# Kernel optimization log

Hardware: AMD Instinct MI355X
Metric: run time of the kernel (lower is better)

Reference implementation:

```python
import jax, jax.numpy as jnp
import numpy as np

BN_EPS = 1e-5


def _bn(x, g, b, m, v):
    # inference-mode BatchNorm2d over channel axis 1 of [B,C,F,T]
    scale = (g * jax.lax.rsqrt(v + BN_EPS))[None, :, None, None]
    shift = (b - g * m * jax.lax.rsqrt(v + BN_EPS))[None, :, None, None]
    return x * scale + shift


def _prelu(x, a):
    return jnp.where(x > 0, x, a[None, :, None, None] * x)


def _conv1x1(x, w):
    # w: [out, in]; x: [B,C,F,T]
    return jnp.einsum('oc,bcft->boft', w, x)


def setup_inputs() -> dict:
    key = jax.random.key(0)
    ks = jax.random.split(key, 8)
    B, C, F, T = 4, 64, 256, 400
    d_c = C // 4  # 16
    inp = jax.random.normal(ks[0], (B, C, F, T), dtype=jnp.float32)
    # causal time mask: True = masked (future frames)
    mask = jnp.triu(jnp.ones((T, T), dtype=bool), k=1)[None, None]  # [1,1,T,T]
    w_fqkv = jax.random.normal(ks[1], (3 * d_c, C), dtype=jnp.float32) / np.sqrt(C)
    w_tqk = jax.random.normal(ks[2], (2 * d_c, C), dtype=jnp.float32) / np.sqrt(C)
    w_proj = jax.random.normal(ks[3], (C, d_c), dtype=jnp.float32) / np.sqrt(d_c)
    def bn_params(k, n):
        k1, k2 = jax.random.split(k)
        return (1.0 + 0.1 * jax.random.normal(k1, (n,), dtype=jnp.float32),
                0.1 * jax.random.normal(k2, (n,), dtype=jnp.float32),
                0.1 * jax.random.normal(jax.random.fold_in(k, 7), (n,), dtype=jnp.float32),
                jnp.abs(1.0 + 0.1 * jax.random.normal(jax.random.fold_in(k, 9), (n,), dtype=jnp.float32)))
    g1, b1, m1, v1 = bn_params(ks[4], 3 * d_c)
    g2, b2, m2, v2 = bn_params(ks[5], 2 * d_c)
    g3, b3, m3, v3 = bn_params(ks[6], C)
    a1 = 0.25 * jnp.ones((3 * d_c,), dtype=jnp.float32)
    a2 = 0.25 * jnp.ones((2 * d_c,), dtype=jnp.float32)
    a3 = 0.25 * jnp.ones((C,), dtype=jnp.float32)
    return dict(inp=inp, mask=mask, w_fqkv=w_fqkv, g1=g1, b1=b1, m1=m1, v1=v1, a1=a1,
                w_tqk=w_tqk, g2=g2, b2=b2, m2=m2, v2=v2, a2=a2,
                w_proj=w_proj, g3=g3, b3=b3, m3=m3, v3=v3, a3=a3)


def reference(inp, mask, w_fqkv, g1, b1, m1, v1, a1,
              w_tqk, g2, b2, m2, v2, a2,
              w_proj, g3, b3, m3, v3, a3):
    d_c = w_proj.shape[1]
    scale = 1.0 / np.sqrt(d_c).astype(np.float32)
    # frequency attention
    f_qkv = _prelu(_bn(_conv1x1(inp, w_fqkv), g1, b1, m1, v1), a1)  # [B,3d,F,T]
    qf, kf, v = f_qkv[:, :d_c], f_qkv[:, d_c:2 * d_c], f_qkv[:, 2 * d_c:]
    f_score = jnp.einsum('bcft,bcyt->btfy', qf, kf) * scale
    f_score = jax.nn.softmax(f_score, axis=-1)
    f_out = jnp.einsum('btfy,bcyt->bcft', f_score, v)
    # time attention
    t_qk = _prelu(_bn(_conv1x1(inp, w_tqk), g2, b2, m2, v2), a2)  # [B,2d,F,T]
    qt, kt = t_qk[:, :d_c], t_qk[:, d_c:]
    t_score = jnp.einsum('bcft,bcfy->bfty', qt, kt) * scale
    neg = -jnp.finfo(t_score.dtype).max
    t_score = jnp.where(mask, neg, t_score)
    t_score = jax.nn.softmax(t_score, axis=-1)
    t_out = jnp.einsum('bfty,bcfy->bcft', t_score, f_out)
    out = _prelu(_bn(_conv1x1(t_out, w_proj), g3, b3, m3, v3), a3)
    return out + inp
```

## Files before the change

kernel.cpp:

```cpp
#include <hip/hip_runtime.h>
#include <hip/hip_bf16.h>

#define B_ 4
#define C_ 64
#define F_ 256
#define T_ 400
#define DC 16
#define NB 102400

typedef __hip_bfloat16 bf16;
typedef __attribute__((ext_vector_type(8))) short bf16x8s;
typedef __attribute__((ext_vector_type(4))) short short4v;
typedef __attribute__((ext_vector_type(4))) float f32x4;
typedef __attribute__((ext_vector_type(2))) short short2v;
typedef __attribute__((ext_vector_type(2))) unsigned int uint2v;
typedef __attribute__((ext_vector_type(4))) unsigned int uint4v;

__device__ __forceinline__ float b2f(bf16 x){ return __bfloat162float(x); }
__device__ __forceinline__ bf16  f2b(float x){ return __float2bfloat16(x); }
__device__ __forceinline__ short f2bs(float x){ bf16 h = __float2bfloat16(x); short s; __builtin_memcpy(&s,&h,2); return s; }

#define MFMA16(a,b,c) __builtin_amdgcn_mfma_f32_16x16x32_bf16((a),(b),(c),0,0,0)

__device__ __forceinline__ unsigned cvt_pk_bf16(float a, float b){
    unsigned r;
    asm("v_cvt_pk_bf16_f32 %0, %1, %2" : "=v"(r) : "v"(a), "v"(b));
    return r;
}
__device__ __forceinline__ void permlane32_swap(unsigned &a, unsigned &b){
    asm("v_permlane32_swap_b32 %0, %1" : "+v"(a), "+v"(b));
}
__device__ __forceinline__ void permlane16_swap(unsigned &a, unsigned &b){
    asm("v_permlane16_swap_b32 %0, %1" : "+v"(a), "+v"(b));
}

__global__ __launch_bounds__(256) void k_proj(
    const float* __restrict__ inp,
    const float* __restrict__ w_fqkv,
    const float* __restrict__ g1, const float* __restrict__ b1,
    const float* __restrict__ m1, const float* __restrict__ v1,
    const float* __restrict__ a1,
    const float* __restrict__ w_tqk,
    const float* __restrict__ g2, const float* __restrict__ b2,
    const float* __restrict__ m2, const float* __restrict__ v2,
    const float* __restrict__ a2,
    bf16* __restrict__ qf, bf16* __restrict__ kf, bf16* __restrict__ vv,
    bf16* __restrict__ qt, bf16* __restrict__ kt)
{
    __shared__ short Xs[256*64];
    __shared__ short Ws[80*72];
    __shared__ float sc[80], sh[80], al[80];

    const int tid = threadIdx.x;
    const int blk = blockIdx.x;
    const int b   = blk / 400;
    const int rem = blk - b*400;
    const int f0  = (rem & 15) * 16;
    const int t0  = (rem >> 4) * 16;

    for (int i = tid; i < 80*32; i += 256) {
        int o = i >> 5, cp = (i & 31) * 2;
        const float* src = (o < 48) ? &w_fqkv[o*64 + cp] : &w_tqk[(o-48)*64 + cp];
        short2v wv; wv.x = f2bs(src[0]); wv.y = f2bs(src[1]);
        *(short2v*)&Ws[o*72 + cp] = wv;
    }
    if (tid < 48) {
        float rs = rsqrtf(v1[tid] + 1e-5f);
        float g  = g1[tid];
        sc[tid] = g * rs;
        sh[tid] = b1[tid] - g * m1[tid] * rs;
        al[tid] = a1[tid];
    }
    if (tid >= 128 && tid < 160) {
        int o = tid - 128;
        float rs = rsqrtf(v2[o] + 1e-5f);
        float g  = g2[o];
        sc[48+o] = g * rs;
        sh[48+o] = b2[o] - g * m2[o] * rs;
        al[48+o] = a2[o];
    }
    {
        const int wv = tid >> 6, lnn = tid & 63;
        const int fi = lnn >> 2, tc = lnn & 3;
        const float* xb = inp + (size_t)b*64*NB + (size_t)(f0+fi)*T_ + t0 + tc*4;
        #pragma unroll
        for (int p = 0; p < 16; p++) {
            const int c = p*4 + wv;
            f32x4 x = *(const f32x4*)&xb[(size_t)c*NB];
            const int chi = c >> 3, clo = c & 7;
            #pragma unroll
            for (int j = 0; j < 4; j++) {
                int r = (tc*4 + j)*16 + fi;
                int slot = chi ^ (r & 7) ^ ((r >> 4) & 7);
                Xs[r*64 + slot*8 + clo] = f2bs(x[j]);
            }
        }
    }
    __syncthreads();

    const int wave = tid >> 6;
    const int lane = tid & 63;
    const int ln   = lane & 15;
    const int quad = lane >> 4;
    const f32x4 zero = {0.f,0.f,0.f,0.f};

    bf16x8s B1[4][2];
    bf16x8s B2[4][2];
    #pragma unroll
    for (int nt = 0; nt < 4; nt++) {
        const int tile = wave*4 + nt;
        {
            const int r  = tile*16 + ln;
            const int sw = (ln & 7) ^ (tile & 7);
            B1[nt][0] = *(const bf16x8s*)&Xs[r*64 + ((quad     ^ sw) * 8)];
            B1[nt][1] = *(const bf16x8s*)&Xs[r*64 + (((4+quad) ^ sw) * 8)];
        }
        {
            const int r  = ln*16 + tile;
            const int sw = (tile & 7) ^ (ln & 7);
            B2[nt][0] = *(const bf16x8s*)&Xs[r*64 + ((quad     ^ sw) * 8)];
            B2[nt][1] = *(const bf16x8s*)&Xs[r*64 + (((4+quad) ^ sw) * 8)];
        }
    }

    #pragma unroll
    for (int mt = 0; mt < 5; mt++) {
        bf16x8s A0 = *(const bf16x8s*)&Ws[(mt*16+ln)*72 + quad*8];
        bf16x8s A1 = *(const bf16x8s*)&Ws[(mt*16+ln)*72 + 32 + quad*8];
        float scv[4], shv[4], alv[4];
        #pragma unroll
        for (int r = 0; r < 4; r++) {
            int o = mt*16 + quad*4 + r;
            scv[r] = sc[o]; shv[r] = sh[o]; alv[r] = al[o];
        }
        #pragma unroll
        for (int nt = 0; nt < 4; nt++) {
            bf16x8s Bb0 = (mt < 3) ? B1[nt][0] : B2[nt][0];
            bf16x8s Bb1 = (mt < 3) ? B1[nt][1] : B2[nt][1];
            f32x4 acc = MFMA16(A0, Bb0, zero);
            acc = MFMA16(A1, Bb1, acc);
            short4v hs;
            #pragma unroll
            for (int r = 0; r < 4; r++) {
                float y = acc[r]*scv[r] + shv[r];
                y = y > 0.f ? y : alv[r]*y;
                if (mt == 0 || mt == 3) y *= 0.25f;
                hs[r] = f2bs(y);
            }
            const int tile = wave*4 + nt;
            if (mt < 3) {
                size_t idx = (((size_t)b*T_ + (t0+tile))*F_ + (f0+ln))*DC + quad*4;
                bf16* dst = (mt == 0) ? qf : (mt == 1) ? kf : vv;
                *(short4v*)((short*)dst + idx) = hs;
            } else {
                size_t idx = (((size_t)b*F_ + (f0+tile))*T_ + (t0+ln))*DC + quad*4;
                bf16* dst = (mt == 3) ? qt : kt;
                *(short4v*)((short*)dst + idx) = hs;
            }
        }
    }
}

__global__ __launch_bounds__(256) void k_fattn(
    const bf16* __restrict__ qf, const bf16* __restrict__ kf,
    const bf16* __restrict__ vv, bf16* __restrict__ fout)
{
    __shared__ short Ks[F_*24];
    __shared__ short Vt[16*264];

    const int bt = blockIdx.x;
    const int b = bt / T_, t = bt - b*T_;
    const size_t base = ((size_t)b*T_ + t)*F_*DC;
    const short* kfp = (const short*)(kf + base);
    const short* vvp = (const short*)(vv + base);
    const short* qfp = (const short*)(qf + base);
    const int tid = threadIdx.x;

    for (int i = tid; i < F_*2; i += 256) {
        int r = i >> 1, cp = (i & 1) * 8;
        *(bf16x8s*)&Ks[r*24+cp] = *(const bf16x8s*)&kfp[r*16+cp];
    }
    for (int i = tid; i < F_; i += 256) {
        bf16x8s v0 = *(const bf16x8s*)&vvp[i*16];
        bf16x8s v1 = *(const bf16x8s*)&vvp[i*16+8];
        #pragma unroll
        for (int c = 0; c < 8; c++) Vt[c*264 + i]     = v0[c];
        #pragma unroll
        for (int c = 0; c < 8; c++) Vt[(8+c)*264 + i] = v1[c];
    }
    __syncthreads();

    const int wave = tid >> 6;
    const int lane = tid & 63;
    const int ln   = lane & 15;
    const int quad = lane >> 4;
    const f32x4 zero = {0.f,0.f,0.f,0.f};

    for (int s = wave; s < F_/16; s += 4) {
        bf16x8s Qf = {};
        if (quad < 2) Qf = *(const bf16x8s*)&qfp[(s*16+ln)*16 + quad*8];

        float ssum = 0.f;
        f32x4 O = zero;
        for (int ch = 0; ch < 4; ch++) {
            unsigned w[4][2];
            #pragma unroll
            for (int i2 = 0; i2 < 4; i2++) {
                int yt = ch*4 + i2;
                bf16x8s Kf = {};
                if (quad < 2) Kf = *(const bf16x8s*)&Ks[(yt*16+ln)*24 + quad*8];
                f32x4 S = MFMA16(Kf, Qf, zero);
                f32x4 p;
                #pragma unroll
                for (int r = 0; r < 4; r++) { p[r] = __expf(S[r]); ssum += p[r]; }
                w[i2][0] = cvt_pk_bf16(p[0], p[1]);
                w[i2][1] = cvt_pk_bf16(p[2], p[3]);
            }
            #pragma unroll
            for (int h = 0; h < 2; h++) {
                unsigned t0a = w[2*h][0],   t0b = w[2*h][1];
                unsigned t1a = w[2*h+1][0], t1b = w[2*h+1][1];
                permlane32_swap(t0a, t1a);
                permlane32_swap(t0b, t1b);
                permlane16_swap(t0a, t1a);
                permlane16_swap(t0b, t1b);
                union { uint4v u; bf16x8s v; } P;
                P.u = (uint4v){t0a, t0b, t1a, t1b};
                bf16x8s Vb = *(const bf16x8s*)&Vt[ln*264 + ch*64 + h*32 + quad*8];
                O = MFMA16(Vb, P.v, O);
            }
        }
        ssum += __shfl_xor(ssum, 16, 64);
        ssum += __shfl_xor(ssum, 32, 64);
        float rinv = __builtin_amdgcn_rcpf(ssum);
        unsigned o0 = cvt_pk_bf16(O[0]*rinv, O[1]*rinv);
        unsigned o1 = cvt_pk_bf16(O[2]*rinv, O[3]*rinv);
        const int f = s*16 + ln;
        *(uint2v*)((short*)fout + (((size_t)b*F_ + f)*T_ + t)*DC + quad*4)
            = (uint2v){o0, o1};
    }
}

__global__ __launch_bounds__(256) void k_tattn(
    const bf16* __restrict__ qt, const bf16* __restrict__ kt,
    const bf16* __restrict__ fo, bf16* __restrict__ tout)
{
    __shared__ short Ks[T_*24];
    __shared__ short Vt[16*456];

    const int bfi = blockIdx.x;
    const int b = bfi / F_, f = bfi - b*F_;
    const size_t base = ((size_t)b*F_ + f)*T_*DC;
    const short* ktp = (const short*)(kt + base);
    const short* fop = (const short*)(fo + base);
    const short* qtp = (const short*)(qt + base);
    const int tid = threadIdx.x;

    for (int i = tid; i < T_*2; i += 256) {
        int r = i >> 1, cp = (i & 1) * 8;
        *(bf16x8s*)&Ks[r*24+cp] = *(const bf16x8s*)&ktp[r*16+cp];
    }
    for (int i = tid; i < T_; i += 256) {
        bf16x8s v0 = *(const bf16x8s*)&fop[i*16];
        bf16x8s v1 = *(const bf16x8s*)&fop[i*16+8];
        #pragma unroll
        for (int c = 0; c < 8; c++) Vt[c*456 + i]     = v0[c];
        #pragma unroll
        for (int c = 0; c < 8; c++) Vt[(8+c)*456 + i] = v1[c];
    }
    for (int i = tid; i < 16*64; i += 256) {
        int c = i >> 6, y = T_ + (i & 63);
        if (y < 456) Vt[c*456 + y] = 0;
    }
    __syncthreads();

    const int wave = tid >> 6;
    const int lane = tid & 63;
    const int ln   = lane & 15;
    const int quad = lane >> 4;
    const f32x4 zero = {0.f,0.f,0.f,0.f};

    unsigned long long sched;
    switch (wave) {
      case 0:  sched = 24ull | (16ull<<5) | (12ull<<10) | ( 8ull<<15) | ( 4ull<<20) | ( 0ull<<25) | ( 3ull<<30); break;
      case 1:  sched = 23ull | (19ull<<5) | (15ull<<10) | (11ull<<15) | ( 7ull<<20) | ( 2ull<<25) | ( 1ull<<30); break;
      case 2:  sched = 22ull | (18ull<<5) | (14ull<<10) | (10ull<<15) | ( 9ull<<20) | ( 5ull<<25) | (31ull<<30); break;
      default: sched = 21ull | (17ull<<5) | (13ull<<10) | (20ull<<15) | ( 6ull<<20) | (31ull<<25) | (31ull<<30); break;
    }

    for (int it = 0; it < 7; it++) {
        const int s = (int)((sched >> (5*it)) & 31);
        if (s == 31) break;

        bf16x8s Qf = {};
        if (quad < 2) Qf = *(const bf16x8s*)&qtp[(s*16+ln)*16 + quad*8];

        float ssum = 0.f;
        f32x4 O = zero;
        const int nch = (s >> 2) + 1;
        for (int ch = 0; ch < nch; ch++) {
            unsigned w[4][2];
            #pragma unroll
            for (int i2 = 0; i2 < 4; i2++) {
                int yt = ch*4 + i2;
                if (yt <= s) {
                    bf16x8s Kf = {};
                    if (quad < 2) Kf = *(const bf16x8s*)&Ks[(yt*16+ln)*24 + quad*8];
                    f32x4 S = MFMA16(Kf, Qf, zero);
                    const bool diag = (yt == s);
                    f32x4 p;
                    #pragma unroll
                    for (int r = 0; r < 4; r++) {
                        p[r] = __expf(S[r]);
                        if (diag && (quad*4 + r > ln)) p[r] = 0.f;
                        ssum += p[r];
                    }
                    w[i2][0] = cvt_pk_bf16(p[0], p[1]);
                    w[i2][1] = cvt_pk_bf16(p[2], p[3]);
                } else {
                    w[i2][0] = 0u; w[i2][1] = 0u;
                }
            }
            #pragma unroll
            for (int h = 0; h < 2; h++) {
                unsigned t0a = w[2*h][0],   t0b = w[2*h][1];
                unsigned t1a = w[2*h+1][0], t1b = w[2*h+1][1];
                permlane32_swap(t0a, t1a);
                permlane32_swap(t0b, t1b);
                permlane16_swap(t0a, t1a);
                permlane16_swap(t0b, t1b);
                union { uint4v u; bf16x8s v; } P;
                P.u = (uint4v){t0a, t0b, t1a, t1b};
                bf16x8s Vb = *(const bf16x8s*)&Vt[ln*456 + ch*64 + h*32 + quad*8];
                O = MFMA16(Vb, P.v, O);
            }
        }
        ssum += __shfl_xor(ssum, 16, 64);
        ssum += __shfl_xor(ssum, 32, 64);
        float rinv = __builtin_amdgcn_rcpf(ssum);
        unsigned o0 = cvt_pk_bf16(O[0]*rinv, O[1]*rinv);
        unsigned o1 = cvt_pk_bf16(O[2]*rinv, O[3]*rinv);
        *(uint2v*)((short*)tout + base + (size_t)(s*16+ln)*DC + quad*4)
            = (uint2v){o0, o1};
    }
}

__global__ __launch_bounds__(256) void k_proj2(
    const bf16* __restrict__ tog, const float* __restrict__ w_proj,
    const float* __restrict__ g3, const float* __restrict__ b3,
    const float* __restrict__ m3, const float* __restrict__ v3,
    const float* __restrict__ a3,
    const float* __restrict__ inp, float* __restrict__ out)
{
    __shared__ short Ws2[64*24];
    __shared__ float sc[64], sh[64], al[64];

    const int tid = threadIdx.x;
    const int b   = blockIdx.x / 400;
    const int n0  = (blockIdx.x - b*400) * 256;

    for (int i = tid; i < 64*8; i += 256) {
        int o = i >> 3, cp = (i & 7) * 2;
        short2v wv; wv.x = f2bs(w_proj[o*16+cp]); wv.y = f2bs(w_proj[o*16+cp+1]);
        *(short2v*)&Ws2[o*24 + cp] = wv;
    }
    if (tid < 64) {
        float rs = rsqrtf(v3[tid] + 1e-5f);
        float g  = g3[tid];
        sc[tid] = g * rs;
        sh[tid] = b3[tid] - g * m3[tid] * rs;
        al[tid] = a3[tid];
    }
    __syncthreads();

    const int wave = tid >> 6;
    const int lane = tid & 63;
    const int ln   = lane & 15;
    const int quad = lane >> 4;
    const f32x4 zero = {0.f,0.f,0.f,0.f};
    const short* top = (const short*)tog + (size_t)b*NB*DC;

    bf16x8s Bf[4];
    #pragma unroll
    for (int nt = 0; nt < 4; nt++) {
        Bf[nt] = (bf16x8s){};
        if (quad < 2) {
            int n = n0 + wave*64 + nt*16 + ln;
            Bf[nt] = *(const bf16x8s*)&top[(size_t)n*DC + quad*8];
        }
    }

    #pragma unroll
    for (int mt = 0; mt < 4; mt++) {
        bf16x8s A = {};
        if (quad < 2) A = *(const bf16x8s*)&Ws2[(mt*16+ln)*24 + quad*8];
        float scv[4], shv[4], alv[4];
        #pragma unroll
        for (int r = 0; r < 4; r++) {
            int o = mt*16 + quad*4 + r;
            scv[r] = sc[o]; shv[r] = sh[o]; alv[r] = al[o];
        }
        #pragma unroll
        for (int nt = 0; nt < 4; nt++) {
            f32x4 acc = MFMA16(A, Bf[nt], zero);
            const int n = n0 + wave*64 + nt*16 + ln;
            #pragma unroll
            for (int r = 0; r < 4; r++) {
                int o = mt*16 + quad*4 + r;
                float y = acc[r]*scv[r] + shv[r];
                y = y > 0.f ? y : alv[r]*y;
                size_t gi = ((size_t)b*64 + o)*NB + n;
                out[gi] = y + inp[gi];
            }
        }
    }
}

extern "C" void kernel_launch(void* const* d_in, const int* in_sizes, int n_in,
                              void* d_out, int out_size, void* d_ws, size_t ws_size,
                              hipStream_t stream)
{
    const float* inp    = (const float*)d_in[0];
    const float* w_fqkv = (const float*)d_in[2];
    const float* g1 = (const float*)d_in[3],  *b1 = (const float*)d_in[4];
    const float* m1 = (const float*)d_in[5],  *v1 = (const float*)d_in[6];
    const float* a1 = (const float*)d_in[7];
    const float* w_tqk  = (const float*)d_in[8];
    const float* g2 = (const float*)d_in[9],  *b2 = (const float*)d_in[10];
    const float* m2 = (const float*)d_in[11], *v2 = (const float*)d_in[12];
    const float* a2 = (const float*)d_in[13];
    const float* w_proj = (const float*)d_in[14];
    const float* g3 = (const float*)d_in[15], *b3 = (const float*)d_in[16];
    const float* m3 = (const float*)d_in[17], *v3 = (const float*)d_in[18];
    const float* a3 = (const float*)d_in[19];
    float* out = (float*)d_out;

    const size_t NQ = (size_t)B_*T_*F_*DC;
    bf16* ws = (bf16*)d_ws;
    bf16 *qf = ws,        *kf = ws + NQ,   *vv = ws + 2*NQ;
    bf16 *qt = ws + 3*NQ, *kt = ws + 4*NQ;
    bf16 *fo = ws + 5*NQ, *to = ws + 6*NQ;

    k_proj <<<B_*400, 256, 0, stream>>>(inp, w_fqkv, g1,b1,m1,v1,a1,
                                        w_tqk, g2,b2,m2,v2,a2,
                                        qf, kf, vv, qt, kt);
    k_fattn<<<B_*T_, 256, 0, stream>>>(qf, kf, vv, fo);
    k_tattn<<<B_*F_, 256, 0, stream>>>(qt, kt, fo, to);
    k_proj2<<<B_*400, 256, 0, stream>>>(to, w_proj, g3,b3,m3,v3,a3, inp, out);
}
```

Measured before the change: 342.5 us.

## Stage projection input via global_load_lds in two channel halves with packed bf16 conversion

The projection kernel now loads its fp32 input tile straight into an LDS staging buffer with global_load_lds DMA, in two halves of 32 channels each. Each thread converts eight channels at once with v_cvt_pk_bf16 and writes one 16-byte swizzled store, replacing many scalar bf16 LDS stores. The second half's DMA is issued before the first half's B fragments are read, so the load overlaps that work. In exchange it adds about 32KB of LDS, which can reduce blocks per CU, plus extra barriers.

```diff
diff --git a/kernel.cpp b/kernel.cpp
--- a/kernel.cpp
+++ b/kernel.cpp
@@ -32,6 +32,12 @@
 }
 __device__ __forceinline__ void permlane16_swap(unsigned &a, unsigned &b){
     asm("v_permlane16_swap_b32 %0, %1" : "+v"(a), "+v"(b));
+}
+
+typedef __attribute__((address_space(3))) unsigned lds_u32;
+typedef __attribute__((address_space(1))) const unsigned glb_u32;
+__device__ __forceinline__ void dma16(const void* g, void* l){
+    __builtin_amdgcn_global_load_lds((glb_u32*)g, (lds_u32*)l, 16, 0, 0);
 }
 
 __global__ __launch_bounds__(256) void k_proj(
@@ -47,6 +53,7 @@
     bf16* __restrict__ qf, bf16* __restrict__ kf, bf16* __restrict__ vv,
     bf16* __restrict__ qt, bf16* __restrict__ kt)
 {
+    __shared__ float Xf[32*256];
     __shared__ short Xs[256*64];
     __shared__ short Ws[80*72];
     __shared__ float sc[80], sh[80], al[80];
@@ -58,11 +65,22 @@
     const int f0  = (rem & 15) * 16;
     const int t0  = (rem >> 4) * 16;
 
+    const int wv  = tid >> 6;
+    const int lnn = tid & 63;
+    const int fi  = lnn >> 2, tq = lnn & 3;
+    const float* gbase = inp + (size_t)b*64*NB + (size_t)(f0+fi)*T_ + t0 + tq*4;
+
+    #pragma unroll
+    for (int i = 0; i < 8; i++) {
+        const int cl = wv*8 + i;
+        dma16(gbase + (size_t)cl*NB, &Xf[cl*256]);
+    }
+
     for (int i = tid; i < 80*32; i += 256) {
         int o = i >> 5, cp = (i & 31) * 2;
         const float* src = (o < 48) ? &w_fqkv[o*64 + cp] : &w_tqk[(o-48)*64 + cp];
-        short2v wv; wv.x = f2bs(src[0]); wv.y = f2bs(src[1]);
-        *(short2v*)&Ws[o*72 + cp] = wv;
+        short2v wvv; wvv.x = f2bs(src[0]); wvv.y = f2bs(src[1]);
+        *(short2v*)&Ws[o*72 + cp] = wvv;
     }
     if (tid < 48) {
         float rs = rsqrtf(v1[tid] + 1e-5f);
@@ -79,26 +97,33 @@
         sh[48+o] = b2[o] - g * m2[o] * rs;
         al[48+o] = a2[o];
     }
+    __syncthreads();
+
     {
-        const int wv = tid >> 6, lnn = tid & 63;
-        const int fi = lnn >> 2, tc = lnn & 3;
-        const float* xb = inp + (size_t)b*64*NB + (size_t)(f0+fi)*T_ + t0 + tc*4;
-        #pragma unroll
-        for (int p = 0; p < 16; p++) {
-            const int c = p*4 + wv;
-            f32x4 x = *(const f32x4*)&xb[(size_t)c*NB];
-            const int chi = c >> 3, clo = c & 7;
-            #pragma unroll
-            for (int j = 0; j < 4; j++) {
-                int r = (tc*4 + j)*16 + fi;
-                int slot = chi ^ (r & 7) ^ ((r >> 4) & 7);
-                Xs[r*64 + slot*8 + clo] = f2bs(x[j]);
-            }
-        }
-    }
-    __syncthreads();
-
-    const int wave = tid >> 6;
+        f32x4 xc[8];
+        #pragma unroll
+        for (int cc = 0; cc < 8; cc++)
+            xc[cc] = *(const f32x4*)&Xf[(wv*8+cc)*256 + fi*16 + tq*4];
+        #pragma unroll
+        for (int j = 0; j < 4; j++) {
+            const int p    = (tq*4+j)*16 + fi;
+            const int slot = (0*4 + wv) ^ (fi&7) ^ ((tq*4+j)&7);
+            union { unsigned u[4]; bf16x8s v; } pk;
+            pk.u[0] = cvt_pk_bf16(xc[0][j], xc[1][j]);
+            pk.u[1] = cvt_pk_bf16(xc[2][j], xc[3][j]);
+            pk.u[2] = cvt_pk_bf16(xc[4][j], xc[5][j]);
+            pk.u[3] = cvt_pk_bf16(xc[6][j], xc[7][j]);
+            *(bf16x8s*)&Xs[p*64 + slot*8] = pk.v;
+        }
+    }
+    __syncthreads();
+
+    #pragma unroll
+    for (int i = 0; i < 8; i++) {
+        const int cl = wv*8 + i;
+        dma16(gbase + (size_t)(32 + cl)*NB, &Xf[cl*256]);
+    }
+
     const int lane = tid & 63;
     const int ln   = lane & 15;
     const int quad = lane >> 4;
@@ -108,17 +133,50 @@
     bf16x8s B2[4][2];
     #pragma unroll
     for (int nt = 0; nt < 4; nt++) {
-        const int tile = wave*4 + nt;
+        const int tile = wv*4 + nt;
         {
             const int r  = tile*16 + ln;
             const int sw = (ln & 7) ^ (tile & 7);
-            B1[nt][0] = *(const bf16x8s*)&Xs[r*64 + ((quad     ^ sw) * 8)];
-            B1[nt][1] = *(const bf16x8s*)&Xs[r*64 + (((4+quad) ^ sw) * 8)];
+            B1[nt][0] = *(const bf16x8s*)&Xs[r*64 + ((quad ^ sw) * 8)];
         }
         {
             const int r  = ln*16 + tile;
             const int sw = (tile & 7) ^ (ln & 7);
-            B2[nt][0] = *(const bf16x8s*)&Xs[r*64 + ((quad     ^ sw) * 8)];
+            B2[nt][0] = *(const bf16x8s*)&Xs[r*64 + ((quad ^ sw) * 8)];
+        }
+    }
+    __syncthreads();
+
+    {
+        f32x4 xc[8];
+        #pragma unroll
+        for (int cc = 0; cc < 8; cc++)
+            xc[cc] = *(const f32x4*)&Xf[(wv*8+cc)*256 + fi*16 + tq*4];
+        #pragma unroll
+        for (int j = 0; j < 4; j++) {
+            const int p    = (tq*4+j)*16 + fi;
+            const int slot = (1*4 + wv) ^ (fi&7) ^ ((tq*4+j)&7);
+            union { unsigned u[4]; bf16x8s v; } pk;
+            pk.u[0] = cvt_pk_bf16(xc[0][j], xc[1][j]);
+            pk.u[1] = cvt_pk_bf16(xc[2][j], xc[3][j]);
+            pk.u[2] = cvt_pk_bf16(xc[4][j], xc[5][j]);
+            pk.u[3] = cvt_pk_bf16(xc[6][j], xc[7][j]);
+            *(bf16x8s*)&Xs[p*64 + slot*8] = pk.v;
+        }
+    }
+    __syncthreads();
+
+    #pragma unroll
+    for (int nt = 0; nt < 4; nt++) {
+        const int tile = wv*4 + nt;
+        {
+            const int r  = tile*16 + ln;
+            const int sw = (ln & 7) ^ (tile & 7);
+            B1[nt][1] = *(const bf16x8s*)&Xs[r*64 + (((4+quad) ^ sw) * 8)];
+        }
+        {
+            const int r  = ln*16 + tile;
+            const int sw = (tile & 7) ^ (ln & 7);
             B2[nt][1] = *(const bf16x8s*)&Xs[r*64 + (((4+quad) ^ sw) * 8)];
         }
     }
@@ -147,7 +205,7 @@
                 if (mt == 0 || mt == 3) y *= 0.25f;
                 hs[r] = f2bs(y);
             }
-            const int tile = wave*4 + nt;
+            const int tile = wv*4 + nt;
             if (mt < 3) {
                 size_t idx = (((size_t)b*T_ + (t0+tile))*F_ + (f0+ln))*DC + quad*4;
                 bf16* dst = (mt == 0) ? qf : (mt == 1) ? kf : vv;
```

New measurement: 348.3 us. Within noise of the previous version (+1.7%).

## Make k_proj persistent over time tiles with register-prefetched input

Applied to the files above, without the earlier changes.

k_proj now launches 512 blocks, each looping over 3-4 consecutive 16-step time tiles for one (batch, frequency-slab), instead of one block per tile. While the MFMA projection of the current tile runs, the next tile's fp32 input is prefetched into registers. Conversion to bf16 is done with packed cvt instructions and 16-byte LDS stores using a changed channel-to-wave assignment. The weight and BN setup is amortised across tiles and load latency is hidden behind compute. The costs are higher register pressure (launch bounds now ask for 3 blocks per CU) and fewer blocks for the scheduler to balance.

```diff
diff --git a/kernel.cpp b/kernel.cpp
--- a/kernel.cpp
+++ b/kernel.cpp
@@ -34,7 +34,7 @@
     asm("v_permlane16_swap_b32 %0, %1" : "+v"(a), "+v"(b));
 }
 
-__global__ __launch_bounds__(256) void k_proj(
+__global__ __launch_bounds__(256, 3) void k_proj(
     const float* __restrict__ inp,
     const float* __restrict__ w_fqkv,
     const float* __restrict__ g1, const float* __restrict__ b1,
@@ -53,16 +53,27 @@
 
     const int tid = threadIdx.x;
     const int blk = blockIdx.x;
-    const int b   = blk / 400;
-    const int rem = blk - b*400;
-    const int f0  = (rem & 15) * 16;
-    const int t0  = (rem >> 4) * 16;
+    const int b   = blk >> 7;
+    const int rem = blk & 127;
+    const int fs  = rem >> 3;
+    const int seg = rem & 7;
+    const int f0  = fs * 16;
+    const int st0 = (seg == 0) ? 0 : (3*seg + 1);
+    const int cnt = (seg == 0) ? 4 : 3;
+
+    const int wv  = tid >> 6;
+    const int lnn = tid & 63;
+    const int fi  = lnn >> 2, tq = lnn & 3;
+    const int lane = lnn;
+    const int ln   = lane & 15;
+    const int quad = lane >> 4;
+    const f32x4 zero = {0.f,0.f,0.f,0.f};
 
     for (int i = tid; i < 80*32; i += 256) {
         int o = i >> 5, cp = (i & 31) * 2;
         const float* src = (o < 48) ? &w_fqkv[o*64 + cp] : &w_tqk[(o-48)*64 + cp];
-        short2v wv; wv.x = f2bs(src[0]); wv.y = f2bs(src[1]);
-        *(short2v*)&Ws[o*72 + cp] = wv;
+        short2v wvv; wvv.x = f2bs(src[0]); wvv.y = f2bs(src[1]);
+        *(short2v*)&Ws[o*72 + cp] = wvv;
     }
     if (tid < 48) {
         float rs = rsqrtf(v1[tid] + 1e-5f);
@@ -79,85 +90,95 @@
         sh[48+o] = b2[o] - g * m2[o] * rs;
         al[48+o] = a2[o];
     }
-    {
-        const int wv = tid >> 6, lnn = tid & 63;
-        const int fi = lnn >> 2, tc = lnn & 3;
-        const float* xb = inp + (size_t)b*64*NB + (size_t)(f0+fi)*T_ + t0 + tc*4;
-        #pragma unroll
-        for (int p = 0; p < 16; p++) {
-            const int c = p*4 + wv;
-            f32x4 x = *(const f32x4*)&xb[(size_t)c*NB];
-            const int chi = c >> 3, clo = c & 7;
-            #pragma unroll
-            for (int j = 0; j < 4; j++) {
-                int r = (tc*4 + j)*16 + fi;
-                int slot = chi ^ (r & 7) ^ ((r >> 4) & 7);
-                Xs[r*64 + slot*8 + clo] = f2bs(x[j]);
-            }
-        }
-    }
-    __syncthreads();
-
-    const int wave = tid >> 6;
-    const int lane = tid & 63;
-    const int ln   = lane & 15;
-    const int quad = lane >> 4;
-    const f32x4 zero = {0.f,0.f,0.f,0.f};
-
-    bf16x8s B1[4][2];
-    bf16x8s B2[4][2];
+
+    const float* xb0 = inp + (size_t)b*64*NB + (size_t)(f0+fi)*T_ + tq*4;
+    int t0 = st0 * 16;
+    f32x4 X[16];
     #pragma unroll
-    for (int nt = 0; nt < 4; nt++) {
-        const int tile = wave*4 + nt;
-        {
-            const int r  = tile*16 + ln;
-            const int sw = (ln & 7) ^ (tile & 7);
-            B1[nt][0] = *(const bf16x8s*)&Xs[r*64 + ((quad     ^ sw) * 8)];
-            B1[nt][1] = *(const bf16x8s*)&Xs[r*64 + (((4+quad) ^ sw) * 8)];
-        }
-        {
-            const int r  = ln*16 + tile;
-            const int sw = (tile & 7) ^ (ln & 7);
-            B2[nt][0] = *(const bf16x8s*)&Xs[r*64 + ((quad     ^ sw) * 8)];
-            B2[nt][1] = *(const bf16x8s*)&Xs[r*64 + (((4+quad) ^ sw) * 8)];
-        }
-    }
-
-    #pragma unroll
-    for (int mt = 0; mt < 5; mt++) {
-        bf16x8s A0 = *(const bf16x8s*)&Ws[(mt*16+ln)*72 + quad*8];
-        bf16x8s A1 = *(const bf16x8s*)&Ws[(mt*16+ln)*72 + 32 + quad*8];
-        float scv[4], shv[4], alv[4];
-        #pragma unroll
-        for (int r = 0; r < 4; r++) {
-            int o = mt*16 + quad*4 + r;
-            scv[r] = sc[o]; shv[r] = sh[o]; alv[r] = al[o];
-        }
+    for (int cc = 0; cc < 16; cc++)
+        X[cc] = *(const f32x4*)&xb0[(size_t)(wv*16+cc)*NB + t0];
+
+    for (int k = 0; k < cnt; k++, t0 += 16) {
+        #pragma unroll
+        for (int j = 0; j < 4; j++) {
+            const int p    = (tq*4+j)*16 + fi;
+            const int gbit = (fi & 7) ^ ((tq*4 + j) & 7);
+            union { unsigned u[4]; bf16x8s v; } pk0, pk1;
+            pk0.u[0] = cvt_pk_bf16(X[0][j],  X[1][j]);
+            pk0.u[1] = cvt_pk_bf16(X[2][j],  X[3][j]);
+            pk0.u[2] = cvt_pk_bf16(X[4][j],  X[5][j]);
+            pk0.u[3] = cvt_pk_bf16(X[6][j],  X[7][j]);
+            pk1.u[0] = cvt_pk_bf16(X[8][j],  X[9][j]);
+            pk1.u[1] = cvt_pk_bf16(X[10][j], X[11][j]);
+            pk1.u[2] = cvt_pk_bf16(X[12][j], X[13][j]);
+            pk1.u[3] = cvt_pk_bf16(X[14][j], X[15][j]);
+            *(bf16x8s*)&Xs[p*64 + ((wv*2    ) ^ gbit)*8] = pk0.v;
+            *(bf16x8s*)&Xs[p*64 + ((wv*2 + 1) ^ gbit)*8] = pk1.v;
+        }
+        __syncthreads();
+
+        bf16x8s B1[4][2];
+        bf16x8s B2[4][2];
         #pragma unroll
         for (int nt = 0; nt < 4; nt++) {
-            bf16x8s Bb0 = (mt < 3) ? B1[nt][0] : B2[nt][0];
-            bf16x8s Bb1 = (mt < 3) ? B1[nt][1] : B2[nt][1];
-            f32x4 acc = MFMA16(A0, Bb0, zero);
-            acc = MFMA16(A1, Bb1, acc);
-            short4v hs;
+            const int tile = wv*4 + nt;
+            {
+                const int r  = tile*16 + ln;
+                const int sw = (ln & 7) ^ (tile & 7);
+                B1[nt][0] = *(const bf16x8s*)&Xs[r*64 + ((quad     ^ sw) * 8)];
+                B1[nt][1] = *(const bf16x8s*)&Xs[r*64 + (((4+quad) ^ sw) * 8)];
+            }
+            {
+                const int r  = ln*16 + tile;
+                const int sw = (tile & 7) ^ (ln & 7);
+                B2[nt][0] = *(const bf16x8s*)&Xs[r*64 + ((quad     ^ sw) * 8)];
+                B2[nt][1] = *(const bf16x8s*)&Xs[r*64 + (((4+quad) ^ sw) * 8)];
+            }
+        }
+
+        if (k + 1 < cnt) {
+            #pragma unroll
+            for (int cc = 0; cc < 16; cc++)
+                X[cc] = *(const f32x4*)&xb0[(size_t)(wv*16+cc)*NB + t0 + 16];
+        }
+
+        #pragma unroll
+        for (int mt = 0; mt < 5; mt++) {
+            bf16x8s A0 = *(const bf16x8s*)&Ws[(mt*16+ln)*72 + quad*8];
+            bf16x8s A1 = *(const bf16x8s*)&Ws[(mt*16+ln)*72 + 32 + quad*8];
+            float scv[4], shv[4], alv[4];
             #pragma unroll
             for (int r = 0; r < 4; r++) {
-                float y = acc[r]*scv[r] + shv[r];
-                y = y > 0.f ? y : alv[r]*y;
-                if (mt == 0 || mt == 3) y *= 0.25f;
-                hs[r] = f2bs(y);
-            }
-            const int tile = wave*4 + nt;
-            if (mt < 3) {
-                size_t idx = (((size_t)b*T_ + (t0+tile))*F_ + (f0+ln))*DC + quad*4;
-                bf16* dst = (mt == 0) ? qf : (mt == 1) ? kf : vv;
-                *(short4v*)((short*)dst + idx) = hs;
-            } else {
-                size_t idx = (((size_t)b*F_ + (f0+tile))*T_ + (t0+ln))*DC + quad*4;
-                bf16* dst = (mt == 3) ? qt : kt;
-                *(short4v*)((short*)dst + idx) = hs;
-            }
-        }
+                int o = mt*16 + quad*4 + r;
+                scv[r] = sc[o]; shv[r] = sh[o]; alv[r] = al[o];
+            }
+            #pragma unroll
+            for (int nt = 0; nt < 4; nt++) {
+                bf16x8s Bb0 = (mt < 3) ? B1[nt][0] : B2[nt][0];
+                bf16x8s Bb1 = (mt < 3) ? B1[nt][1] : B2[nt][1];
+                f32x4 acc = MFMA16(A0, Bb0, zero);
+                acc = MFMA16(A1, Bb1, acc);
+                short4v hs;
+                #pragma unroll
+                for (int r = 0; r < 4; r++) {
+                    float y = acc[r]*scv[r] + shv[r];
+                    y = y > 0.f ? y : alv[r]*y;
+                    if (mt == 0 || mt == 3) y *= 0.25f;
+                    hs[r] = f2bs(y);
+                }
+                const int tile = wv*4 + nt;
+                if (mt < 3) {
+                    size_t idx = (((size_t)b*T_ + (t0+tile))*F_ + (f0+ln))*DC + quad*4;
+                    bf16* dst = (mt == 0) ? qf : (mt == 1) ? kf : vv;
+                    *(short4v*)((short*)dst + idx) = hs;
+                } else {
+                    size_t idx = (((size_t)b*F_ + (f0+tile))*T_ + (t0+ln))*DC + quad*4;
+                    bf16* dst = (mt == 3) ? qt : kt;
+                    *(short4v*)((short*)dst + idx) = hs;
+                }
+            }
+        }
+        __syncthreads();
     }
 }
 
@@ -441,9 +462,9 @@
     bf16 *qt = ws + 3*NQ, *kt = ws + 4*NQ;
     bf16 *fo = ws + 5*NQ, *to = ws + 6*NQ;
 
-    k_proj <<<B_*400, 256, 0, stream>>>(inp, w_fqkv, g1,b1,m1,v1,a1,
-                                        w_tqk, g2,b2,m2,v2,a2,
-                                        qf, kf, vv, qt, kt);
+    k_proj <<<512, 256, 0, stream>>>(inp, w_fqkv, g1,b1,m1,v1,a1,
+                                     w_tqk, g2,b2,m2,v2,a2,
+                                     qf, kf, vv, qt, kt);
     k_fattn<<<B_*T_, 256, 0, stream>>>(qf, kf, vv, fo);
     k_tattn<<<B_*F_, 256, 0, stream>>>(qt, kt, fo, to);
     k_proj2<<<B_*400, 256, 0, stream>>>(to, w_proj, g3,b3,m3,v3,a3, inp, out);
```

Result: slower. 394.5 us (+15.2%).
